# Kernel tuning notes

Measured on AMD Instinct MI355X. Metric: run time of the kernel, lower is better.

## Reference

```python
import jax, jax.numpy as jnp
import numpy as np

B, N, D = 256, 64, 128
E, K, T = 8, 2, 80
H = 2 * D  # expert hidden


def setup_inputs() -> dict:
    key = jax.random.key(0)
    ks = jax.random.split(key, 4)
    s = 1.0 / np.sqrt(D)
    return {
        "x": jax.random.normal(ks[0], (B, N, D), dtype=jnp.float32),
        "router_w": jax.random.normal(ks[1], (D, E), dtype=jnp.float32) * s,
        "router_b": jnp.zeros((E,), dtype=jnp.float32),
        "w1": jax.random.normal(ks[2], (E, D, H), dtype=jnp.float32) * s,
        "b1": jnp.zeros((E, H), dtype=jnp.float32),
        "w2": jax.random.normal(ks[3], (E, H, T * 2), dtype=jnp.float32) * (1.0 / np.sqrt(H)),
        "b2": jnp.zeros((E, T * 2), dtype=jnp.float32),
        "A": N,
    }


def reference(x, router_w, router_b, w1, b1, w2, b2, A):
    k = K
    xa = x[:, 1:A]                                   # [B, A-1, D] agents w/o ego
    # --- router: per-sample logits -> softmax -> top-k gates ---
    pooled = xa.mean(axis=1)                         # [B, D]
    logits = pooled @ router_w + router_b            # [B, E]
    probs = jax.nn.softmax(logits, axis=-1)
    topk_probs, topk_idx = jax.lax.top_k(probs, k)   # [B, k]
    # dense gate matrix: sum_k p_k * onehot(idx_k)
    gates = jnp.sum(jax.nn.one_hot(topk_idx, E, dtype=probs.dtype)
                    * topk_probs[..., None], axis=1)  # [B, E]
    # --- experts: per-agent MLP, all experts batched (grouped GEMM form) ---
    h = jax.nn.relu(jnp.einsum('bnd,edh->ebnh', xa, w1) + b1[:, None, None, :])
    out_e = jnp.einsum('ebnh,eho->ebno', h, w2) + b2[:, None, None, :]  # [E,B,A-1,T*2]
    out_e = out_e.reshape(E, out_e.shape[1], out_e.shape[2], T, 2)
    # --- weighted combine (scatter-combine expressed densely) ---
    output = jnp.einsum('be,ebntc->bntc', gates, out_e)  # [B, A-1, T, 2]
    return output
```

## Files before the change

kernel.cpp:

```cpp
#include <hip/hip_runtime.h>
#include <hip/hip_bf16.h>

#define B_   256
#define N_   64
#define D_   128
#define E_   8
#define T_   80
#define H_   256
#define O_   160
#define NTOK 63

typedef __bf16 bf16x8 __attribute__((ext_vector_type(8)));
typedef float  f32x4  __attribute__((ext_vector_type(4)));
typedef unsigned short u16x8 __attribute__((ext_vector_type(8)));
typedef unsigned short u16x4 __attribute__((ext_vector_type(4)));

__device__ __forceinline__ unsigned short f2bf(float f) {
    unsigned int u = __builtin_bit_cast(unsigned int, f);
    u += 0x7FFFu + ((u >> 16) & 1u);
    return (unsigned short)(u >> 16);
}

__global__ __launch_bounds__(256)
void prep_w(const float* __restrict__ w1, const float* __restrict__ w2,
            unsigned short* __restrict__ w1t, unsigned short* __restrict__ w2t) {
    __shared__ float tile[32][33];
    const int bid = blockIdx.x;
    const int t = threadIdx.x;
    const int r  = t >> 3;
    const int c4 = (t & 7) * 4;

    const float* src; unsigned short* dst;
    int src_ld, dst_ld;
    size_t soff, doff;
    if (bid < 256) {
        int e = bid >> 5, rest = bid & 31;
        int dt = rest >> 3, ht = rest & 7;
        soff = ((size_t)e * 128 + dt * 32) * 256 + ht * 32; src_ld = 256;
        doff = ((size_t)e * 256 + ht * 32) * 128 + dt * 32; dst_ld = 128;
        src = w1; dst = w1t;
    } else {
        int id = bid - 256;
        int e = id / 40, rest = id % 40;
        int ht = rest / 5, ot = rest % 5;
        soff = ((size_t)e * 256 + ht * 32) * 160 + ot * 32; src_ld = 160;
        doff = ((size_t)e * 160 + ot * 32) * 256 + ht * 32; dst_ld = 256;
        src = w2; dst = w2t;
    }
    float4 v = *(const float4*)(src + soff + (size_t)r * src_ld + c4);
    tile[r][c4 + 0] = v.x; tile[r][c4 + 1] = v.y;
    tile[r][c4 + 2] = v.z; tile[r][c4 + 3] = v.w;
    __syncthreads();
    const int c  = t >> 3;
    const int r4 = (t & 7) * 4;
    u16x4 h4;
    h4[0] = f2bf(tile[r4 + 0][c]); h4[1] = f2bf(tile[r4 + 1][c]);
    h4[2] = f2bf(tile[r4 + 2][c]); h4[3] = f2bf(tile[r4 + 3][c]);
    *(u16x4*)(dst + doff + (size_t)c * dst_ld + r4) = h4;
}

__global__ __launch_bounds__(512)
void moe_fused(const float* __restrict__ x,
               const float* __restrict__ rw,
               const float* __restrict__ rb,
               const float* __restrict__ b1,
               const float* __restrict__ b2,
               const unsigned short* __restrict__ w1t,
               const unsigned short* __restrict__ w2t,
               float* __restrict__ out) {
    const int b    = blockIdx.x;
    const int t    = threadIdx.x;
    const int wv   = t >> 6;
    const int lane = t & 63;
    const int wvM  = wv >> 2;
    const int wvN  = wv & 3;
    const int q    = lane >> 4;
    const int r16  = lane & 15;

    __shared__ unsigned short xa_lds[64 * 128];
    __shared__ unsigned short h_lds[64 * 256];
    __shared__ float part[16][128];
    __shared__ float pooled[128];
    __shared__ int   re_s[2];
    __shared__ float rg_s[2];

    {
        const int rbase = t >> 5;
        const int c0    = (t & 31) * 4;
        float4 ps = make_float4(0.f, 0.f, 0.f, 0.f);
        const float* xb = x + ((size_t)b * N_ + 1) * D_;
        #pragma unroll
        for (int rr = 0; rr < 4; ++rr) {
            int row = rbase + rr * 16;
            float4 v = make_float4(0.f, 0.f, 0.f, 0.f);
            if (row < NTOK) v = *(const float4*)(xb + (size_t)row * D_ + c0);
            ps.x += v.x; ps.y += v.y; ps.z += v.z; ps.w += v.w;
            u16x4 h4;
            h4[0] = f2bf(v.x); h4[1] = f2bf(v.y);
            h4[2] = f2bf(v.z); h4[3] = f2bf(v.w);
            *(u16x4*)&xa_lds[row * 128 + (c0 ^ ((row & 7) << 3))] = h4;
        }
        *(float4*)&part[rbase][c0] = ps;
    }
    __syncthreads();

    if (t < 128) {
        float s = 0.f;
        #pragma unroll
        for (int i = 0; i < 16; ++i) s += part[i][t];
        pooled[t] = s * (1.f / 63.f);
    }
    __syncthreads();

    if (t < 64) {
        int e  = lane >> 3;
        int dg = lane & 7;
        float p = 0.f;
        #pragma unroll
        for (int i = 0; i < 16; ++i)
            p += pooled[dg * 16 + i] * rw[(dg * 16 + i) * E_ + e];
        p += __shfl_xor(p, 1); p += __shfl_xor(p, 2); p += __shfl_xor(p, 4);
        float lg[E_];
        #pragma unroll
        for (int e2 = 0; e2 < E_; ++e2) lg[e2] = __shfl(p, e2 * 8) + rb[e2];
        if (lane == 0) {
            float mx = lg[0];
            for (int i = 1; i < E_; ++i) mx = fmaxf(mx, lg[i]);
            float pr[E_]; float den = 0.f;
            for (int i = 0; i < E_; ++i) { pr[i] = expf(lg[i] - mx); den += pr[i]; }
            int i0 = 0;
            for (int i = 1; i < E_; ++i) if (pr[i] > pr[i0]) i0 = i;
            int i1 = (i0 == 0) ? 1 : 0;
            for (int i = 0; i < E_; ++i) if (i != i0 && pr[i] > pr[i1]) i1 = i;
            float inv = 1.f / den;
            re_s[0] = i0; re_s[1] = i1;
            rg_s[0] = pr[i0] * inv; rg_s[1] = pr[i1] * inv;
        }
    }
    __syncthreads();

    const int   e0 = re_s[0], e1 = re_s[1];
    const float g0 = rg_s[0], g1 = rg_s[1];

    const f32x4 z4 = {0.f, 0.f, 0.f, 0.f};
    f32x4 acc2[2][3];
    #pragma unroll
    for (int mt = 0; mt < 2; ++mt)
        #pragma unroll
        for (int j = 0; j < 3; ++j) acc2[mt][j] = z4;

    #pragma unroll
    for (int s = 0; s < 2; ++s) {
        const int   e = s ? e1 : e0;
        const float g = s ? g1 : g0;
        const unsigned short* w1e = w1t + (size_t)e * H_ * D_;

        f32x4 acc1[2][4];
        #pragma unroll
        for (int mt = 0; mt < 2; ++mt)
            #pragma unroll
            for (int nt = 0; nt < 4; ++nt) acc1[mt][nt] = z4;

        const int row0 = wvM * 32 + r16;
        const int row1 = wvM * 32 + 16 + r16;
        #pragma unroll
        for (int ks = 0; ks < 4; ++ks) {
            int col0k = ks * 32 + q * 8;
            bf16x8 a0 = __builtin_bit_cast(bf16x8,
                *(const u16x8*)&xa_lds[row0 * 128 + (col0k ^ ((row0 & 7) << 3))]);
            bf16x8 a1 = __builtin_bit_cast(bf16x8,
                *(const u16x8*)&xa_lds[row1 * 128 + (col0k ^ ((row1 & 7) << 3))]);
            #pragma unroll
            for (int nt = 0; nt < 4; ++nt) {
                int col = wvN * 64 + nt * 16 + r16;
                bf16x8 bb = __builtin_bit_cast(bf16x8,
                    *(const u16x8*)(w1e + (size_t)col * D_ + col0k));
                acc1[0][nt] = __builtin_amdgcn_mfma_f32_16x16x32_bf16(a0, bb, acc1[0][nt], 0, 0, 0);
                acc1[1][nt] = __builtin_amdgcn_mfma_f32_16x16x32_bf16(a1, bb, acc1[1][nt], 0, 0, 0);
            }
        }

        if (s == 1) __syncthreads();

        float b1v[4];
        #pragma unroll
        for (int nt = 0; nt < 4; ++nt) b1v[nt] = b1[e * H_ + wvN * 64 + nt * 16 + r16];
        #pragma unroll
        for (int mt = 0; mt < 2; ++mt)
            #pragma unroll
            for (int nt = 0; nt < 4; ++nt) {
                int col = wvN * 64 + nt * 16 + r16;
                #pragma unroll
                for (int rg = 0; rg < 4; ++rg) {
                    int row = wvM * 32 + mt * 16 + q * 4 + rg;
                    float v = acc1[mt][nt][rg] + b1v[nt];
                    v = fmaxf(v, 0.f) * g;
                    h_lds[row * 256 + (col ^ ((row & 7) << 3))] = f2bf(v);
                }
            }
        __syncthreads();

        const unsigned short* w2e = w2t + (size_t)e * O_ * H_;
        #pragma unroll
        for (int ks = 0; ks < 8; ++ks) {
            int col0k = ks * 32 + q * 8;
            bf16x8 a0 = __builtin_bit_cast(bf16x8,
                *(const u16x8*)&h_lds[row0 * 256 + (col0k ^ ((row0 & 7) << 3))]);
            bf16x8 a1 = __builtin_bit_cast(bf16x8,
                *(const u16x8*)&h_lds[row1 * 256 + (col0k ^ ((row1 & 7) << 3))]);
            #pragma unroll
            for (int j = 0; j < 3; ++j) {
                int nt2 = wvN + j * 4;
                if (nt2 < 10) {
                    int col = nt2 * 16 + r16;
                    bf16x8 bb = __builtin_bit_cast(bf16x8,
                        *(const u16x8*)(w2e + (size_t)col * H_ + col0k));
                    acc2[0][j] = __builtin_amdgcn_mfma_f32_16x16x32_bf16(a0, bb, acc2[0][j], 0, 0, 0);
                    acc2[1][j] = __builtin_amdgcn_mfma_f32_16x16x32_bf16(a1, bb, acc2[1][j], 0, 0, 0);
                }
            }
        }
    }

    #pragma unroll
    for (int j = 0; j < 3; ++j) {
        int nt2 = wvN + j * 4;
        if (nt2 < 10) {
            int col = nt2 * 16 + r16;
            float bias = g0 * b2[e0 * O_ + col] + g1 * b2[e1 * O_ + col];
            #pragma unroll
            for (int mt = 0; mt < 2; ++mt)
                #pragma unroll
                for (int rg = 0; rg < 4; ++rg) {
                    int n = wvM * 32 + mt * 16 + q * 4 + rg;
                    if (n < NTOK)
                        out[((size_t)b * NTOK + n) * O_ + col] = acc2[mt][j][rg] + bias;
                }
        }
    }
}

extern "C" void kernel_launch(void* const* d_in, const int* in_sizes, int n_in,
                              void* d_out, int out_size, void* d_ws, size_t ws_size,
                              hipStream_t stream) {
    const float* x  = (const float*)d_in[0];
    const float* rw = (const float*)d_in[1];
    const float* rb = (const float*)d_in[2];
    const float* w1 = (const float*)d_in[3];
    const float* b1 = (const float*)d_in[4];
    const float* w2 = (const float*)d_in[5];
    const float* b2 = (const float*)d_in[6];
    float* out = (float*)d_out;

    unsigned short* w1t = (unsigned short*)d_ws;
    unsigned short* w2t = w1t + (size_t)E_ * H_ * D_;

    prep_w<<<576, 256, 0, stream>>>(w1, w2, w1t, w2t);
    moe_fused<<<B_, 512, 0, stream>>>(x, rw, rb, b1, b2, w1t, w2t, out);
}
```

Measured before the change: 99.34 us.

## Move routing into prep kernel and split each sample across two blocks

```diff
diff --git a/kernel.cpp b/kernel.cpp
--- a/kernel.cpp
+++ b/kernel.cpp
@@ -15,6 +15,8 @@
 typedef unsigned short u16x8 __attribute__((ext_vector_type(8)));
 typedef unsigned short u16x4 __attribute__((ext_vector_type(4)));
 
+struct Route { int e0, e1; float g0, g1; };
+
 __device__ __forceinline__ unsigned short f2bf(float f) {
     unsigned int u = __builtin_bit_cast(unsigned int, f);
     u += 0x7FFFu + ((u >> 16) & 1u);
@@ -22,125 +24,137 @@
 }
 
 __global__ __launch_bounds__(256)
-void prep_w(const float* __restrict__ w1, const float* __restrict__ w2,
-            unsigned short* __restrict__ w1t, unsigned short* __restrict__ w2t) {
-    __shared__ float tile[32][33];
+void prep_route(const float* __restrict__ x,
+                const float* __restrict__ rw,
+                const float* __restrict__ rb,
+                const float* __restrict__ w1,
+                const float* __restrict__ w2,
+                unsigned short* __restrict__ w1t,
+                unsigned short* __restrict__ w2t,
+                Route* __restrict__ rt) {
+    __shared__ float smem[1184];
     const int bid = blockIdx.x;
     const int t = threadIdx.x;
-    const int r  = t >> 3;
-    const int c4 = (t & 7) * 4;
-
-    const float* src; unsigned short* dst;
-    int src_ld, dst_ld;
-    size_t soff, doff;
-    if (bid < 256) {
-        int e = bid >> 5, rest = bid & 31;
-        int dt = rest >> 3, ht = rest & 7;
-        soff = ((size_t)e * 128 + dt * 32) * 256 + ht * 32; src_ld = 256;
-        doff = ((size_t)e * 256 + ht * 32) * 128 + dt * 32; dst_ld = 128;
-        src = w1; dst = w1t;
+
+    if (bid < 576) {
+        const int r  = t >> 3;
+        const int c4 = (t & 7) * 4;
+        const float* src; unsigned short* dst;
+        int src_ld, dst_ld;
+        size_t soff, doff;
+        if (bid < 256) {
+            int e = bid >> 5, rest = bid & 31;
+            int dt = rest >> 3, ht = rest & 7;
+            soff = ((size_t)e * 128 + dt * 32) * 256 + ht * 32; src_ld = 256;
+            doff = ((size_t)e * 256 + ht * 32) * 128 + dt * 32; dst_ld = 128;
+            src = w1; dst = w1t;
+        } else {
+            int id = bid - 256;
+            int e = id / 40, rest = id % 40;
+            int ht = rest / 5, ot = rest % 5;
+            soff = ((size_t)e * 256 + ht * 32) * 160 + ot * 32; src_ld = 160;
+            doff = ((size_t)e * 160 + ot * 32) * 256 + ht * 32; dst_ld = 256;
+            src = w2; dst = w2t;
+        }
+        float4 v = *(const float4*)(src + soff + (size_t)r * src_ld + c4);
+        smem[r * 33 + c4 + 0] = v.x; smem[r * 33 + c4 + 1] = v.y;
+        smem[r * 33 + c4 + 2] = v.z; smem[r * 33 + c4 + 3] = v.w;
+        __syncthreads();
+        const int c  = t >> 3;
+        const int r4 = (t & 7) * 4;
+        u16x4 h4;
+        h4[0] = f2bf(smem[(r4 + 0) * 33 + c]); h4[1] = f2bf(smem[(r4 + 1) * 33 + c]);
+        h4[2] = f2bf(smem[(r4 + 2) * 33 + c]); h4[3] = f2bf(smem[(r4 + 3) * 33 + c]);
+        *(u16x4*)(dst + doff + (size_t)c * dst_ld + r4) = h4;
     } else {
-        int id = bid - 256;
-        int e = id / 40, rest = id % 40;
-        int ht = rest / 5, ot = rest % 5;
-        soff = ((size_t)e * 256 + ht * 32) * 160 + ot * 32; src_ld = 160;
-        doff = ((size_t)e * 160 + ot * 32) * 256 + ht * 32; dst_ld = 256;
-        src = w2; dst = w2t;
-    }
-    float4 v = *(const float4*)(src + soff + (size_t)r * src_ld + c4);
-    tile[r][c4 + 0] = v.x; tile[r][c4 + 1] = v.y;
-    tile[r][c4 + 2] = v.z; tile[r][c4 + 3] = v.w;
-    __syncthreads();
-    const int c  = t >> 3;
-    const int r4 = (t & 7) * 4;
-    u16x4 h4;
-    h4[0] = f2bf(tile[r4 + 0][c]); h4[1] = f2bf(tile[r4 + 1][c]);
-    h4[2] = f2bf(tile[r4 + 2][c]); h4[3] = f2bf(tile[r4 + 3][c]);
-    *(u16x4*)(dst + doff + (size_t)c * dst_ld + r4) = h4;
-}
-
-__global__ __launch_bounds__(512)
-void moe_fused(const float* __restrict__ x,
-               const float* __restrict__ rw,
-               const float* __restrict__ rb,
-               const float* __restrict__ b1,
-               const float* __restrict__ b2,
-               const unsigned short* __restrict__ w1t,
-               const unsigned short* __restrict__ w2t,
-               float* __restrict__ out) {
-    const int b    = blockIdx.x;
+        const int b = bid - 576;
+        float* part = smem;
+        float* pooled = smem + 1024;
+        const int c4 = (t & 31) * 4;
+        const int rr = t >> 5;
+        const float* xb = x + ((size_t)b * N_ + 1) * D_;
+        float4 ps = make_float4(0.f, 0.f, 0.f, 0.f);
+        for (int row = rr; row < NTOK; row += 8) {
+            float4 v = *(const float4*)(xb + (size_t)row * D_ + c4);
+            ps.x += v.x; ps.y += v.y; ps.z += v.z; ps.w += v.w;
+        }
+        *(float4*)&part[rr * 128 + c4] = ps;
+        __syncthreads();
+        if (t < 128) {
+            float s = 0.f;
+            #pragma unroll
+            for (int i = 0; i < 8; ++i) s += part[i * 128 + t];
+            pooled[t] = s * (1.f / 63.f);
+        }
+        __syncthreads();
+        if (t < 64) {
+            int e  = t >> 3;
+            int dg = t & 7;
+            float p = 0.f;
+            #pragma unroll
+            for (int i = 0; i < 16; ++i)
+                p += pooled[dg * 16 + i] * rw[(dg * 16 + i) * E_ + e];
+            p += __shfl_xor(p, 1); p += __shfl_xor(p, 2); p += __shfl_xor(p, 4);
+            float lg[E_];
+            #pragma unroll
+            for (int e2 = 0; e2 < E_; ++e2) lg[e2] = __shfl(p, e2 * 8) + rb[e2];
+            if (t == 0) {
+                float mx = lg[0];
+                for (int i = 1; i < E_; ++i) mx = fmaxf(mx, lg[i]);
+                float pr[E_]; float den = 0.f;
+                for (int i = 0; i < E_; ++i) { pr[i] = expf(lg[i] - mx); den += pr[i]; }
+                int i0 = 0;
+                for (int i = 1; i < E_; ++i) if (pr[i] > pr[i0]) i0 = i;
+                int i1 = (i0 == 0) ? 1 : 0;
+                for (int i = 0; i < E_; ++i) if (i != i0 && pr[i] > pr[i1]) i1 = i;
+                float inv = 1.f / den;
+                Route r; r.e0 = i0; r.e1 = i1;
+                r.g0 = pr[i0] * inv; r.g1 = pr[i1] * inv;
+                rt[b] = r;
+            }
+        }
+    }
+}
+
+__global__ __launch_bounds__(256)
+void moe_main(const float* __restrict__ x,
+              const float* __restrict__ b1,
+              const float* __restrict__ b2,
+              const unsigned short* __restrict__ w1t,
+              const unsigned short* __restrict__ w2t,
+              const Route* __restrict__ rt,
+              float* __restrict__ out) {
+    const int half = blockIdx.x;
+    const int b    = blockIdx.y;
+    const int m0   = half * 32;
     const int t    = threadIdx.x;
     const int wv   = t >> 6;
     const int lane = t & 63;
-    const int wvM  = wv >> 2;
-    const int wvN  = wv & 3;
     const int q    = lane >> 4;
     const int r16  = lane & 15;
 
-    __shared__ unsigned short xa_lds[64 * 128];
-    __shared__ unsigned short h_lds[64 * 256];
-    __shared__ float part[16][128];
-    __shared__ float pooled[128];
-    __shared__ int   re_s[2];
-    __shared__ float rg_s[2];
+    __shared__ unsigned short xa_lds[32 * 128];
+    __shared__ unsigned short h_lds[32 * 256];
+
+    const Route rr = rt[b];
 
     {
-        const int rbase = t >> 5;
-        const int c0    = (t & 31) * 4;
-        float4 ps = make_float4(0.f, 0.f, 0.f, 0.f);
-        const float* xb = x + ((size_t)b * N_ + 1) * D_;
-        #pragma unroll
-        for (int rr = 0; rr < 4; ++rr) {
-            int row = rbase + rr * 16;
-            float4 v = make_float4(0.f, 0.f, 0.f, 0.f);
-            if (row < NTOK) v = *(const float4*)(xb + (size_t)row * D_ + c0);
-            ps.x += v.x; ps.y += v.y; ps.z += v.z; ps.w += v.w;
+        int row  = t >> 3;
+        int col0 = (t & 7) * 16;
+        int n = m0 + row;
+        bool valid = (n < NTOK);
+        const float* src = x + ((size_t)b * N_ + (1 + n)) * D_ + col0;
+        #pragma unroll
+        for (int c = 0; c < 4; ++c) {
+            float4 v;
+            if (valid) v = *(const float4*)(src + c * 4);
+            else       v = make_float4(0.f, 0.f, 0.f, 0.f);
             u16x4 h4;
-            h4[0] = f2bf(v.x); h4[1] = f2bf(v.y);
-            h4[2] = f2bf(v.z); h4[3] = f2bf(v.w);
-            *(u16x4*)&xa_lds[row * 128 + (c0 ^ ((row & 7) << 3))] = h4;
-        }
-        *(float4*)&part[rbase][c0] = ps;
-    }
-    __syncthreads();
-
-    if (t < 128) {
-        float s = 0.f;
-        #pragma unroll
-        for (int i = 0; i < 16; ++i) s += part[i][t];
-        pooled[t] = s * (1.f / 63.f);
-    }
-    __syncthreads();
-
-    if (t < 64) {
-        int e  = lane >> 3;
-        int dg = lane & 7;
-        float p = 0.f;
-        #pragma unroll
-        for (int i = 0; i < 16; ++i)
-            p += pooled[dg * 16 + i] * rw[(dg * 16 + i) * E_ + e];
-        p += __shfl_xor(p, 1); p += __shfl_xor(p, 2); p += __shfl_xor(p, 4);
-        float lg[E_];
-        #pragma unroll
-        for (int e2 = 0; e2 < E_; ++e2) lg[e2] = __shfl(p, e2 * 8) + rb[e2];
-        if (lane == 0) {
-            float mx = lg[0];
-            for (int i = 1; i < E_; ++i) mx = fmaxf(mx, lg[i]);
-            float pr[E_]; float den = 0.f;
-            for (int i = 0; i < E_; ++i) { pr[i] = expf(lg[i] - mx); den += pr[i]; }
-            int i0 = 0;
-            for (int i = 1; i < E_; ++i) if (pr[i] > pr[i0]) i0 = i;
-            int i1 = (i0 == 0) ? 1 : 0;
-            for (int i = 0; i < E_; ++i) if (i != i0 && pr[i] > pr[i1]) i1 = i;
-            float inv = 1.f / den;
-            re_s[0] = i0; re_s[1] = i1;
-            rg_s[0] = pr[i0] * inv; rg_s[1] = pr[i1] * inv;
-        }
-    }
-    __syncthreads();
-
-    const int   e0 = re_s[0], e1 = re_s[1];
-    const float g0 = rg_s[0], g1 = rg_s[1];
+            h4[0] = f2bf(v.x); h4[1] = f2bf(v.y); h4[2] = f2bf(v.z); h4[3] = f2bf(v.w);
+            int col = col0 + c * 4;
+            *(u16x4*)&xa_lds[row * 128 + (col ^ ((row & 7) << 3))] = h4;
+        }
+    }
 
     const f32x4 z4 = {0.f, 0.f, 0.f, 0.f};
     f32x4 acc2[2][3];
@@ -149,10 +163,12 @@
         #pragma unroll
         for (int j = 0; j < 3; ++j) acc2[mt][j] = z4;
 
+    __syncthreads();
+
     #pragma unroll
     for (int s = 0; s < 2; ++s) {
-        const int   e = s ? e1 : e0;
-        const float g = s ? g1 : g0;
+        const int   e = s ? rr.e1 : rr.e0;
+        const float g = s ? rr.g1 : rr.g0;
         const unsigned short* w1e = w1t + (size_t)e * H_ * D_;
 
         f32x4 acc1[2][4];
@@ -161,18 +177,17 @@
             #pragma unroll
             for (int nt = 0; nt < 4; ++nt) acc1[mt][nt] = z4;
 
-        const int row0 = wvM * 32 + r16;
-        const int row1 = wvM * 32 + 16 + r16;
         #pragma unroll
         for (int ks = 0; ks < 4; ++ks) {
             int col0k = ks * 32 + q * 8;
+            int row0 = r16, row1 = 16 + r16;
             bf16x8 a0 = __builtin_bit_cast(bf16x8,
                 *(const u16x8*)&xa_lds[row0 * 128 + (col0k ^ ((row0 & 7) << 3))]);
             bf16x8 a1 = __builtin_bit_cast(bf16x8,
                 *(const u16x8*)&xa_lds[row1 * 128 + (col0k ^ ((row1 & 7) << 3))]);
             #pragma unroll
             for (int nt = 0; nt < 4; ++nt) {
-                int col = wvN * 64 + nt * 16 + r16;
+                int col = wv * 64 + nt * 16 + r16;
                 bf16x8 bb = __builtin_bit_cast(bf16x8,
                     *(const u16x8*)(w1e + (size_t)col * D_ + col0k));
                 acc1[0][nt] = __builtin_amdgcn_mfma_f32_16x16x32_bf16(a0, bb, acc1[0][nt], 0, 0, 0);
@@ -184,15 +199,15 @@
 
         float b1v[4];
         #pragma unroll
-        for (int nt = 0; nt < 4; ++nt) b1v[nt] = b1[e * H_ + wvN * 64 + nt * 16 + r16];
+        for (int nt = 0; nt < 4; ++nt) b1v[nt] = b1[e * H_ + wv * 64 + nt * 16 + r16];
         #pragma unroll
         for (int mt = 0; mt < 2; ++mt)
             #pragma unroll
             for (int nt = 0; nt < 4; ++nt) {
-                int col = wvN * 64 + nt * 16 + r16;
+                int col = wv * 64 + nt * 16 + r16;
                 #pragma unroll
                 for (int rg = 0; rg < 4; ++rg) {
-                    int row = wvM * 32 + mt * 16 + q * 4 + rg;
+                    int row = mt * 16 + q * 4 + rg;
                     float v = acc1[mt][nt][rg] + b1v[nt];
                     v = fmaxf(v, 0.f) * g;
                     h_lds[row * 256 + (col ^ ((row & 7) << 3))] = f2bf(v);
@@ -204,13 +219,14 @@
         #pragma unroll
         for (int ks = 0; ks < 8; ++ks) {
             int col0k = ks * 32 + q * 8;
+            int row0 = r16, row1 = 16 + r16;
             bf16x8 a0 = __builtin_bit_cast(bf16x8,
                 *(const u16x8*)&h_lds[row0 * 256 + (col0k ^ ((row0 & 7) << 3))]);
             bf16x8 a1 = __builtin_bit_cast(bf16x8,
                 *(const u16x8*)&h_lds[row1 * 256 + (col0k ^ ((row1 & 7) << 3))]);
             #pragma unroll
             for (int j = 0; j < 3; ++j) {
-                int nt2 = wvN + j * 4;
+                int nt2 = wv + j * 4;
                 if (nt2 < 10) {
                     int col = nt2 * 16 + r16;
                     bf16x8 bb = __builtin_bit_cast(bf16x8,
@@ -224,15 +240,16 @@
 
     #pragma unroll
     for (int j = 0; j < 3; ++j) {
-        int nt2 = wvN + j * 4;
+        int nt2 = wv + j * 4;
         if (nt2 < 10) {
             int col = nt2 * 16 + r16;
-            float bias = g0 * b2[e0 * O_ + col] + g1 * b2[e1 * O_ + col];
+            float bias = rr.g0 * b2[rr.e0 * O_ + col] + rr.g1 * b2[rr.e1 * O_ + col];
             #pragma unroll
             for (int mt = 0; mt < 2; ++mt)
                 #pragma unroll
                 for (int rg = 0; rg < 4; ++rg) {
-                    int n = wvM * 32 + mt * 16 + q * 4 + rg;
+                    int row = mt * 16 + q * 4 + rg;
+                    int n = m0 + row;
                     if (n < NTOK)
                         out[((size_t)b * NTOK + n) * O_ + col] = acc2[mt][j][rg] + bias;
                 }
@@ -254,7 +271,8 @@
 
     unsigned short* w1t = (unsigned short*)d_ws;
     unsigned short* w2t = w1t + (size_t)E_ * H_ * D_;
-
-    prep_w<<<576, 256, 0, stream>>>(w1, w2, w1t, w2t);
-    moe_fused<<<B_, 512, 0, stream>>>(x, rw, rb, b1, b2, w1t, w2t, out);
-}
+    Route* rt = (Route*)(w2t + (size_t)E_ * O_ * H_);
+
+    prep_route<<<832, 256, 0, stream>>>(x, rw, rb, w1, w2, w1t, w2t, rt);
+    moe_main<<<dim3(2, B_), 256, 0, stream>>>(x, b1, b2, w1t, w2t, rt, out);
+}
```

New measurement: 103.8 us. +4.5%, slower.
